# Optimization experiments

Hardware: AMD Instinct MI355X
Metric: run time of the kernel (lower is better)

Reference implementation:

```python
import jax, jax.numpy as jnp
import numpy as np

B, S, E = 2, 2048, 2048
NH, NKV, HD = 32, 8, 64
GS = NH // NKV  # group size = 4
EPS = 1e-6
ROPE_THETA = 10000.0


def setup_inputs() -> dict:
    key = jax.random.key(0)
    ks = jax.random.split(key, 6)
    x = jax.random.normal(ks[0], (B, S, E), jnp.float32)
    position_ids = jnp.broadcast_to(jnp.arange(S, dtype=jnp.int32), (B, S))
    # causal additive mask [1,1,S,S]
    causal = jnp.tril(jnp.ones((S, S), jnp.bool_))
    attn_mask = jnp.where(causal, 0.0, -1e9).astype(jnp.float32)[None, None]
    sc = 0.02
    Wq = jax.random.normal(ks[1], (E, NH * HD), jnp.float32) * sc
    Wk = jax.random.normal(ks[2], (E, NKV * HD), jnp.float32) * sc
    Wv = jax.random.normal(ks[3], (E, NKV * HD), jnp.float32) * sc
    Wo = jax.random.normal(ks[4], (NH * HD, E), jnp.float32) * sc
    q_norm_w = jnp.ones((HD,), jnp.float32)
    k_norm_w = jnp.ones((HD,), jnp.float32)
    return {"x": x, "position_ids": position_ids, "attn_mask": attn_mask,
            "Wq": Wq, "Wk": Wk, "Wv": Wv, "Wo": Wo,
            "q_norm_w": q_norm_w, "k_norm_w": k_norm_w}


def rms_norm(x, w):
    dt = x.dtype
    xf = x.astype(jnp.float32)
    xf = xf * jax.lax.rsqrt(jnp.mean(xf * xf, axis=-1, keepdims=True) + EPS)
    return w * xf.astype(dt)


def apply_rope(x, position_ids):
    # x: [B, H, S, D]; rotate-half RoPE
    D = x.shape[-1]
    inv_freq = 1.0 / (ROPE_THETA ** (jnp.arange(0, D, 2, dtype=jnp.float32) / D))
    freqs = position_ids.astype(jnp.float32)[:, :, None] * inv_freq  # [B,S,D/2]
    cos = jnp.cos(freqs)[:, None]  # [B,1,S,D/2]
    sin = jnp.sin(freqs)[:, None]
    x1, x2 = x[..., : D // 2], x[..., D // 2 :]
    return jnp.concatenate([x1 * cos - x2 * sin, x2 * cos + x1 * sin], axis=-1).astype(x.dtype)


def reference(x, position_ids, attn_mask, Wq, Wk, Wv, Wo, q_norm_w, k_norm_w):
    b, s, _ = x.shape
    Q = (x @ Wq).reshape(b, s, NH, HD).transpose(0, 2, 1, 3)   # [B,NH,S,D]
    K = (x @ Wk).reshape(b, s, NKV, HD).transpose(0, 2, 1, 3)  # [B,NKV,S,D]
    V = (x @ Wv).reshape(b, s, NKV, HD).transpose(0, 2, 1, 3)
    Q = rms_norm(Q, q_norm_w)
    K = rms_norm(K, k_norm_w)
    Q = apply_rope(Q, position_ids)
    K = apply_rope(K, position_ids)
    new_kv_cache = (K, V)
    # GQA: head h attends with kv group h // GS == reshape heads -> (NKV, GS)
    Qg = Q.reshape(b, NKV, GS, s, HD)
    scores = jnp.einsum('bgqsd,bgtd->bgqst', Qg, K) / np.float32(np.sqrt(HD))
    scores = scores + attn_mask[:, :, None]  # broadcast over group dim
    attn = jax.nn.softmax(scores.astype(jnp.float32), axis=-1).astype(x.dtype)
    ctx = jnp.einsum('bgqst,bgtd->bgqsd', attn, V)             # [B,NKV,GS,S,D]
    ctx = ctx.reshape(b, NH, s, HD).transpose(0, 2, 1, 3).reshape(b, s, NH * HD)
    output = ctx @ Wo
    return output, new_kv_cache
```

## Files before the change

### kernel.cpp

```cpp
#include <hip/hip_runtime.h>
#include <stdint.h>

#define S_LEN 2048
#define EMB 2048
#define NHEADS 32
#define NKVH 8
#define HDIM 64

typedef float f32x4 __attribute__((ext_vector_type(4)));
typedef float f32x16 __attribute__((ext_vector_type(16)));
typedef __bf16 bf16x8 __attribute__((ext_vector_type(8)));
typedef unsigned int u32x4 __attribute__((ext_vector_type(4)));

typedef const __attribute__((address_space(1))) void* as1cv;
typedef __attribute__((address_space(3))) void* as3v;

__device__ __forceinline__ void gload_lds16(const void* g, void* l) {
  as1cv gp = (as1cv)(uintptr_t)g;
  as3v lp = (as3v)(uintptr_t)l;
  __builtin_amdgcn_global_load_lds(gp, lp, 16, 0, 0);
}

__device__ __forceinline__ unsigned cvt_pk_bf16(float lo, float hi) {
  unsigned r;
  asm("v_cvt_pk_bf16_f32 %0, %1, %2" : "=v"(r) : "v"(lo), "v"(hi));
  return r;
}

__device__ __forceinline__ void permswap(unsigned& a, unsigned& b) {
  asm("v_permlane32_swap_b32 %0, %1" : "+v"(a), "+v"(b));
}

__device__ __forceinline__ bf16x8 pack4(unsigned a, unsigned b, unsigned c, unsigned d) {
  union { u32x4 u; bf16x8 f; } x;
  x.u = (u32x4){a, b, c, d};
  return x.f;
}

__global__ void rope_table_kernel(float* __restrict__ cosT, float* __restrict__ sinT) {
  int p = blockIdx.x;
  int i = threadIdx.x;
  if (i < 32) {
    float inv = powf(10000.0f, -(float)i / 32.0f);
    float ang = (float)p * inv;
    cosT[p * 32 + i] = cosf(ang);
    sinT[p * 32 + i] = sinf(ang);
  }
}

__global__ __launch_bounds__(256) void cast_bf16_kernel(const float* __restrict__ in,
                                                        __bf16* __restrict__ out, int n8) {
  int i = blockIdx.x * 256 + threadIdx.x;
  if (i < n8) {
    f32x4 a = *(const f32x4*)(in + (size_t)i * 8);
    f32x4 b = *(const f32x4*)(in + (size_t)i * 8 + 4);
    bf16x8 o;
    o[0] = (__bf16)a[0]; o[1] = (__bf16)a[1]; o[2] = (__bf16)a[2]; o[3] = (__bf16)a[3];
    o[4] = (__bf16)b[0]; o[5] = (__bf16)b[1]; o[6] = (__bf16)b[2]; o[7] = (__bf16)b[3];
    *(bf16x8*)(out + (size_t)i * 8) = o;
  }
}

__global__ __launch_bounds__(256) void transpose_cast_kernel(const float* __restrict__ in,
                                                             __bf16* __restrict__ out,
                                                             int R, int C) {
  __shared__ float t[64][65];
  int c0 = blockIdx.x * 64, r0 = blockIdx.y * 64;
  int tid = threadIdx.x;
#pragma unroll
  for (int i = 0; i < 16; ++i) {
    int e = i * 256 + tid;
    int rr = e >> 6, cc = e & 63;
    t[rr][cc] = in[(size_t)(r0 + rr) * C + c0 + cc];
  }
  __syncthreads();
#pragma unroll
  for (int i = 0; i < 16; ++i) {
    int e = i * 256 + tid;
    int rr = e >> 6, cc = e & 63;
    out[(size_t)(c0 + rr) * R + r0 + cc] = (__bf16)t[cc][rr];
  }
}

template <int BM, int BN, typename OUT>
__global__ __launch_bounds__(256, 2) void gemm4w_kernel(const __bf16* __restrict__ A,
                                                        const __bf16* __restrict__ B,
                                                        OUT* __restrict__ C,
                                                        int M, int N, int K) {
  constexpr int MF = (BM / 2) / 16;
  constexpr int NF = (BN / 2) / 16;
  constexpr int ROWS = BM + BN;
  constexpr int NCALL = ROWS / 32;
  constexpr int CHA = BM / 32;
  __shared__ __align__(16) __bf16 sm[2][ROWS * 64];

  const int NT = K >> 6;
  const int nt = N / BN;
  const int nwg = (M / BM) * nt;
  const int q8 = nwg >> 3;
  int wg = blockIdx.x;
  int swz = (wg & 7) * q8 + (wg >> 3);
  int bm = swz / nt, bn = swz % nt;
  size_t m0 = (size_t)bm * BM, n0 = (size_t)bn * BN;

  int tid = threadIdx.x;
  int L = tid & 63, w = tid >> 6;
  int wrow = w >> 1, wcol = w & 1;
  int l15 = L & 15, hi2 = L >> 4;
  int lx = (l15 & 7) << 4;
  const int cx0 = (hi2 << 4) ^ lx;
  const int cx1 = (64 + (hi2 << 4)) ^ lx;

  int srow = tid >> 3;
  int scol = ((tid & 7) ^ (srow & 7)) << 3;
  const __bf16* pA = A + (size_t)(m0 + srow) * K + scol;
  const __bf16* pB = B + (size_t)(n0 + srow) * K + scol;

  char* smb = (char*)sm;
  const int aRow = (wrow * (BM / 2) + l15) * 128;
  const int bRow = (BM + wcol * (BN / 2) + l15) * 128;

  f32x4 acc[MF][NF];
#pragma unroll
  for (int m = 0; m < MF; ++m)
#pragma unroll
    for (int n = 0; n < NF; ++n) acc[m][n] = (f32x4){0.f, 0.f, 0.f, 0.f};

  auto STG = [&](int buf, int c, int t) {
    const __bf16* s = (c < CHA) ? pA + (size_t)(c << 5) * K + ((size_t)t << 6)
                                : pB + (size_t)((c - CHA) << 5) * K + ((size_t)t << 6);
    gload_lds16(s, smb + buf * (ROWS * 128) + c * 4096 + tid * 16);
  };

#pragma unroll
  for (int c = 0; c < NCALL; ++c) STG(0, c, 0);
#pragma unroll
  for (int c = 0; c < NCALL; ++c) STG(1, c, 1);
  if constexpr (NCALL == 10) asm volatile("s_waitcnt vmcnt(10)" ::: "memory");
  else asm volatile("s_waitcnt vmcnt(8)" ::: "memory");
  __builtin_amdgcn_s_barrier();

  for (int t = 0; t < NT; ++t) {
    const char* aC = smb + (t & 1) * (ROWS * 128);
    bf16x8 af[MF][2], bf[NF][2];
#pragma unroll
    for (int n = 0; n < NF; ++n) {
      bf[n][0] = *(const bf16x8*)(aC + bRow + n * 2048 + cx0);
      bf[n][1] = *(const bf16x8*)(aC + bRow + n * 2048 + cx1);
    }
#pragma unroll
    for (int m = 0; m < MF; ++m) {
      af[m][0] = *(const bf16x8*)(aC + aRow + m * 2048 + cx0);
      af[m][1] = *(const bf16x8*)(aC + aRow + m * 2048 + cx1);
    }
    asm volatile("s_waitcnt lgkmcnt(4)" ::: "memory");
    __builtin_amdgcn_sched_barrier(0);
    __builtin_amdgcn_s_setprio(1);
#pragma unroll
    for (int m = 0; m < MF / 2; ++m)
#pragma unroll
      for (int n = 0; n < NF; ++n)
#pragma unroll
        for (int kk = 0; kk < 2; ++kk)
          acc[m][n] = __builtin_amdgcn_mfma_f32_16x16x32_bf16(
              kk ? af[m][1] : af[m][0], kk ? bf[n][1] : bf[n][0], acc[m][n], 0, 0, 0);
    __builtin_amdgcn_s_setprio(0);
    asm volatile("s_waitcnt lgkmcnt(0)" ::: "memory");
    __builtin_amdgcn_sched_barrier(0);
    __builtin_amdgcn_s_barrier();
    if (t + 2 < NT) {
#pragma unroll
      for (int c = 0; c < NCALL; ++c) STG(t & 1, c, t + 2);
    }
    __builtin_amdgcn_s_setprio(1);
#pragma unroll
    for (int m = MF / 2; m < MF; ++m)
#pragma unroll
      for (int n = 0; n < NF; ++n)
#pragma unroll
        for (int kk = 0; kk < 2; ++kk)
          acc[m][n] = __builtin_amdgcn_mfma_f32_16x16x32_bf16(
              kk ? af[m][1] : af[m][0], kk ? bf[n][1] : bf[n][0], acc[m][n], 0, 0, 0);
    __builtin_amdgcn_s_setprio(0);
    if (t + 2 < NT) {
      if constexpr (NCALL == 10) asm volatile("s_waitcnt vmcnt(10)" ::: "memory");
      else asm volatile("s_waitcnt vmcnt(8)" ::: "memory");
    } else if (t + 1 < NT) {
      asm volatile("s_waitcnt vmcnt(0)" ::: "memory");
    }
    __builtin_amdgcn_s_barrier();
  }

#pragma unroll
  for (int m = 0; m < MF; ++m)
#pragma unroll
    for (int n = 0; n < NF; ++n)
#pragma unroll
      for (int r = 0; r < 4; ++r)
        C[(m0 + wrow * (BM / 2) + m * 16 + (hi2 << 2) + r) * (size_t)N + n0 +
          wcol * (BN / 2) + n * 16 + l15] = (OUT)acc[m][n][r];
}

__global__ __launch_bounds__(256) void rmsrope_kernel(
    const __bf16* __restrict__ QKV, const int* __restrict__ pos,
    const float* __restrict__ qw, const float* __restrict__ kw,
    const float* __restrict__ cosT, const float* __restrict__ sinT,
    __bf16* __restrict__ Qatt, __bf16* __restrict__ Katt, __bf16* __restrict__ Vtatt,
    float* __restrict__ Kc, float* __restrict__ Vc) {
  int token = blockIdx.x;
  int b = token >> 11, s = token & 2047;
  int tid = threadIdx.x, lane = tid & 63, wid = tid >> 6;
  int p = pos[token];
  int i = lane & 31;
  float cs = cosT[p * 32 + i], sn = sinT[p * 32 + i];
  const __bf16* base = QKV + (size_t)token * 3072;
  float qwl = qw[lane], kwl = kw[lane];
  const float qscale = 0.18033688011112042f;

  for (int h = wid; h < NHEADS; h += 4) {
    float v = (float)base[h * 64 + lane];
    float ss = v * v;
#pragma unroll
    for (int m = 1; m < 64; m <<= 1) ss += __shfl_xor(ss, m);
    float xn = v * rsqrtf(ss * (1.0f / 64.0f) + 1e-6f) * qwl;
    float other = __shfl_xor(xn, 32);
    float o = xn * cs + ((lane < 32) ? -other * sn : other * sn);
    Qatt[((size_t)(b * NHEADS + h) * S_LEN + s) * HDIM + lane] = (__bf16)(o * qscale);
  }
  for (int g = wid; g < NKVH; g += 4) {
    float v = (float)base[2048 + g * 64 + lane];
    float ss = v * v;
#pragma unroll
    for (int m = 1; m < 64; m <<= 1) ss += __shfl_xor(ss, m);
    float xn = v * rsqrtf(ss * (1.0f / 64.0f) + 1e-6f) * kwl;
    float other = __shfl_xor(xn, 32);
    float o = xn * cs + ((lane < 32) ? -other * sn : other * sn);
    size_t kidx = ((size_t)(b * NKVH + g) * S_LEN + s) * HDIM + lane;
    Katt[kidx] = (__bf16)o;
    Kc[kidx] = o;
  }
  for (int g = wid; g < NKVH; g += 4) {
    float v = (float)base[2560 + g * 64 + lane];
    size_t vidx = ((size_t)(b * NKVH + g) * S_LEN + s) * HDIM + lane;
    Vc[vidx] = v;
    Vtatt[((size_t)(b * NKVH + g) * HDIM + lane) * S_LEN + s] = (__bf16)v;
  }
}

__global__ __launch_bounds__(256, 2) void attn_kernel(const __bf16* __restrict__ Qatt,
                                                      const __bf16* __restrict__ Katt,
                                                      const __bf16* __restrict__ Vtatt,
                                                      __bf16* __restrict__ ctx) {
  __shared__ __align__(16) __bf16 Ks[2][4096];
  __shared__ __align__(16) __bf16 Vs[2][4096];
  int bid = blockIdx.x;
  int qt, bg;
  if (bid < 256) { qt = 31 - (bid >> 4); bg = bid & 15; }
  else { qt = (bid - 256) >> 4; bg = bid & 15; }
  int b = bg >> 3, g = bg & 7;
  int tid = threadIdx.x, lane = tid & 63, w = tid >> 6;
  int l31 = lane & 31, hi = lane >> 5;
  int h = g * 4 + w;

  const __bf16* Kg = Katt + (size_t)bg * (S_LEN * HDIM);
  const __bf16* Vg = Vtatt + (size_t)bg * (HDIM * S_LEN);
  const __bf16* Qg = Qatt + ((size_t)(b * NHEADS + h) * S_LEN + qt * 64 + l31) * HDIM;

  bf16x8 qf0[4], qf1[4];
#pragma unroll
  for (int ds = 0; ds < 4; ++ds) {
    qf0[ds] = *(const bf16x8*)(Qg + ds * 16 + (hi << 3));
    qf1[ds] = *(const bf16x8*)(Qg + 32 * HDIM + ds * 16 + (hi << 3));
  }

  f32x16 acc00, acc01, acc10, acc11;
#pragma unroll
  for (int r = 0; r < 16; ++r) { acc00[r] = 0.f; acc01[r] = 0.f; acc10[r] = 0.f; acc11[r] = 0.f; }
  float l0 = 0.f, l1 = 0.f;

  int sr = tid >> 3;
  int sc = ((tid & 7) ^ (sr & 7)) << 3;
  const __bf16* Ksrc = Kg + (size_t)sr * HDIM + sc;
  const __bf16* Vsrc = Vg + (size_t)sr * S_LEN + sc;

  gload_lds16(Ksrc, &Ks[0][tid * 8]);
  gload_lds16(Ksrc + 32 * HDIM, &Ks[0][2048 + tid * 8]);
  gload_lds16(Vsrc, &Vs[0][tid * 8]);
  gload_lds16(Vsrc + (size_t)32 * S_LEN, &Vs[0][2048 + tid * 8]);
  __syncthreads();

  int rx = (l31 & 7) << 4;

  for (int t = 0; t <= qt; ++t) {
    int cur = t & 1;
    if (t < qt) {
      const __bf16* kn = Ksrc + (size_t)(t + 1) * (64 * HDIM);
      const __bf16* vn = Vsrc + (size_t)(t + 1) * 64;
      gload_lds16(kn, &Ks[cur ^ 1][tid * 8]);
      gload_lds16(kn + 32 * HDIM, &Ks[cur ^ 1][2048 + tid * 8]);
      gload_lds16(vn, &Vs[cur ^ 1][tid * 8]);
      gload_lds16(vn + (size_t)32 * S_LEN, &Vs[cur ^ 1][2048 + tid * 8]);
    }
    f32x16 s00, s01, s10, s11;
#pragma unroll
    for (int r = 0; r < 16; ++r) { s00[r] = 0.f; s01[r] = 0.f; s10[r] = 0.f; s11[r] = 0.f; }
    {
      const char* kb0 = (const char*)Ks[cur] + (size_t)l31 * 128;
      const char* kb1 = kb0 + 4096;
#pragma unroll
      for (int dstep = 0; dstep < 4; ++dstep) {
        int cb = dstep * 32 + (hi << 4);
        bf16x8 k0 = *(const bf16x8*)(kb0 + (cb ^ rx));
        bf16x8 k1 = *(const bf16x8*)(kb1 + (cb ^ rx));
        s00 = __builtin_amdgcn_mfma_f32_32x32x16_bf16(k0, qf0[dstep], s00, 0, 0, 0);
        s01 = __builtin_amdgcn_mfma_f32_32x32x16_bf16(k1, qf0[dstep], s01, 0, 0, 0);
        s10 = __builtin_amdgcn_mfma_f32_32x32x16_bf16(k0, qf1[dstep], s10, 0, 0, 0);
        s11 = __builtin_amdgcn_mfma_f32_32x32x16_bf16(k1, qf1[dstep], s11, 0, 0, 0);
      }
    }
    if (t == qt) {
#pragma unroll
      for (int r = 0; r < 16; ++r) {
        int kb = (r & 3) + 8 * (r >> 2) + (hi << 2);
        if (kb > l31) { s00[r] = -3e38f; s11[r] = -3e38f; }
        s01[r] = -3e38f;
      }
    }
#pragma unroll
    for (int r = 0; r < 16; ++r) {
      s00[r] = __builtin_amdgcn_exp2f(s00[r]);
      s01[r] = __builtin_amdgcn_exp2f(s01[r]);
      s10[r] = __builtin_amdgcn_exp2f(s10[r]);
      s11[r] = __builtin_amdgcn_exp2f(s11[r]);
    }
    {
      float a0 = 0.f, a1 = 0.f, a2 = 0.f, a3 = 0.f;
      float b0 = 0.f, b1 = 0.f, b2 = 0.f, b3 = 0.f;
#pragma unroll
      for (int r = 0; r < 16; r += 4) {
        a0 += s00[r]; a1 += s00[r + 1]; a2 += s00[r + 2]; a3 += s00[r + 3];
        a0 += s01[r]; a1 += s01[r + 1]; a2 += s01[r + 2]; a3 += s01[r + 3];
        b0 += s10[r]; b1 += s10[r + 1]; b2 += s10[r + 2]; b3 += s10[r + 3];
        b0 += s11[r]; b1 += s11[r + 1]; b2 += s11[r + 2]; b3 += s11[r + 3];
      }
      l0 += (a0 + a1) + (a2 + a3);
      l1 += (b0 + b1) + (b2 + b3);
    }
    bf16x8 pf0[4], pf1[4];
    {
      unsigned wd[8];
#pragma unroll
      for (int i = 0; i < 8; ++i) wd[i] = cvt_pk_bf16(s00[2 * i], s00[2 * i + 1]);
      permswap(wd[0], wd[2]); permswap(wd[1], wd[3]);
      permswap(wd[4], wd[6]); permswap(wd[5], wd[7]);
      pf0[0] = pack4(wd[0], wd[1], wd[2], wd[3]);
      pf0[1] = pack4(wd[4], wd[5], wd[6], wd[7]);
#pragma unroll
      for (int i = 0; i < 8; ++i) wd[i] = cvt_pk_bf16(s01[2 * i], s01[2 * i + 1]);
      permswap(wd[0], wd[2]); permswap(wd[1], wd[3]);
      permswap(wd[4], wd[6]); permswap(wd[5], wd[7]);
      pf0[2] = pack4(wd[0], wd[1], wd[2], wd[3]);
      pf0[3] = pack4(wd[4], wd[5], wd[6], wd[7]);
#pragma unroll
      for (int i = 0; i < 8; ++i) wd[i] = cvt_pk_bf16(s10[2 * i], s10[2 * i + 1]);
      permswap(wd[0], wd[2]); permswap(wd[1], wd[3]);
      permswap(wd[4], wd[6]); permswap(wd[5], wd[7]);
      pf1[0] = pack4(wd[0], wd[1], wd[2], wd[3]);
      pf1[1] = pack4(wd[4], wd[5], wd[6], wd[7]);
#pragma unroll
      for (int i = 0; i < 8; ++i) wd[i] = cvt_pk_bf16(s11[2 * i], s11[2 * i + 1]);
      permswap(wd[0], wd[2]); permswap(wd[1], wd[3]);
      permswap(wd[4], wd[6]); permswap(wd[5], wd[7]);
      pf1[2] = pack4(wd[0], wd[1], wd[2], wd[3]);
      pf1[3] = pack4(wd[4], wd[5], wd[6], wd[7]);
    }
    {
      const char* vb0 = (const char*)Vs[cur] + (size_t)l31 * 128;
      const char* vb1 = vb0 + 4096;
#pragma unroll
      for (int ks = 0; ks < 4; ++ks) {
        int cb = ks * 32 + (hi << 4);
        bf16x8 v0 = *(const bf16x8*)(vb0 + (cb ^ rx));
        bf16x8 v1 = *(const bf16x8*)(vb1 + (cb ^ rx));
        acc00 = __builtin_amdgcn_mfma_f32_32x32x16_bf16(v0, pf0[ks], acc00, 0, 0, 0);
        acc01 = __builtin_amdgcn_mfma_f32_32x32x16_bf16(v1, pf0[ks], acc01, 0, 0, 0);
        acc10 = __builtin_amdgcn_mfma_f32_32x32x16_bf16(v0, pf1[ks], acc10, 0, 0, 0);
        acc11 = __builtin_amdgcn_mfma_f32_32x32x16_bf16(v1, pf1[ks], acc11, 0, 0, 0);
      }
    }
    __syncthreads();
  }

  l0 += __shfl_xor(l0, 32);
  l1 += __shfl_xor(l1, 32);
  float inv0 = 1.f / l0, inv1 = 1.f / l1;
  size_t orow0 = ((size_t)(b * S_LEN + qt * 64 + l31)) * EMB + h * HDIM;
  size_t orow1 = orow0 + (size_t)32 * EMB;
#pragma unroll
  for (int r = 0; r < 16; r += 2) {
    int d = (r & 3) + 8 * (r >> 2) + (hi << 2);
    unsigned w00 = cvt_pk_bf16(acc00[r] * inv0, acc00[r + 1] * inv0);
    unsigned w01 = cvt_pk_bf16(acc01[r] * inv0, acc01[r + 1] * inv0);
    unsigned w10 = cvt_pk_bf16(acc10[r] * inv1, acc10[r + 1] * inv1);
    unsigned w11 = cvt_pk_bf16(acc11[r] * inv1, acc11[r + 1] * inv1);
    *(unsigned*)((char*)ctx + (orow0 + d) * 2) = w00;
    *(unsigned*)((char*)ctx + (orow0 + 32 + d) * 2) = w01;
    *(unsigned*)((char*)ctx + (orow1 + d) * 2) = w10;
    *(unsigned*)((char*)ctx + (orow1 + 32 + d) * 2) = w11;
  }
}

extern "C" void kernel_launch(void* const* d_in, const int* in_sizes, int n_in,
                              void* d_out, int out_size, void* d_ws, size_t ws_size,
                              hipStream_t stream) {
  const float* x = (const float*)d_in[0];
  const int* pos = (const int*)d_in[1];
  const float* Wq = (const float*)d_in[3];
  const float* Wk = (const float*)d_in[4];
  const float* Wv = (const float*)d_in[5];
  const float* Wo = (const float*)d_in[6];
  const float* qw = (const float*)d_in[7];
  const float* kw = (const float*)d_in[8];

  float* out = (float*)d_out;
  float* Kc = out + (size_t)2 * 2048 * 2048;
  float* Vc = Kc + (size_t)2 * 8 * 2048 * 64;

  char* ws = (char*)d_ws;
  size_t off = 0;
  auto alloc = [&](size_t bytes) {
    char* p = ws + off;
    off += (bytes + 255) & ~(size_t)255;
    return (void*)p;
  };
  __bf16* xb = (__bf16*)alloc((size_t)4096 * 2048 * 2);
  __bf16* Wcat = (__bf16*)alloc((size_t)3072 * 2048 * 2);
  __bf16* Wot = (__bf16*)alloc((size_t)2048 * 2048 * 2);
  __bf16* QKV = (__bf16*)alloc((size_t)4096 * 3072 * 2);
  __bf16* ctx = (__bf16*)alloc((size_t)4096 * 2048 * 2);
  __bf16* Qatt = (__bf16*)alloc((size_t)2 * 32 * 2048 * 64 * 2);
  __bf16* Katt = (__bf16*)alloc((size_t)2 * 8 * 2048 * 64 * 2);
  __bf16* Vtat = (__bf16*)alloc((size_t)2 * 8 * 2048 * 64 * 2);
  float* cosT = (float*)alloc((size_t)2048 * 32 * 4);
  float* sinT = (float*)alloc((size_t)2048 * 32 * 4);

  rope_table_kernel<<<2048, 64, 0, stream>>>(cosT, sinT);
  cast_bf16_kernel<<<4096, 256, 0, stream>>>(x, xb, 4096 * 2048 / 8);
  transpose_cast_kernel<<<dim3(32, 32), 256, 0, stream>>>(Wq, Wcat, 2048, 2048);
  transpose_cast_kernel<<<dim3(8, 32), 256, 0, stream>>>(Wk, Wcat + (size_t)2048 * 2048, 2048, 512);
  transpose_cast_kernel<<<dim3(8, 32), 256, 0, stream>>>(Wv, Wcat + (size_t)2560 * 2048, 2048, 512);
  transpose_cast_kernel<<<dim3(32, 32), 256, 0, stream>>>(Wo, Wot, 2048, 2048);
  gemm4w_kernel<128, 192, __bf16><<<512, 256, 0, stream>>>(xb, Wcat, QKV, 4096, 3072, 2048);
  rmsrope_kernel<<<4096, 256, 0, stream>>>(QKV, pos, qw, kw, cosT, sinT, Qatt, Katt, Vtat, Kc, Vc);
  attn_kernel<<<512, 256, 0, stream>>>(Qatt, Katt, Vtat, ctx);
  gemm4w_kernel<128, 128, float><<<512, 256, 0, stream>>>(ctx, Wot, out, 4096, 2048, 2048);
}
```

Before: 186.2 us.

## Split long causal attention tiles across two KV chunks with a combine pass

The attention grid grows from 512 to 768 blocks. The 16 longest query tiles per batch-group split their KV range into two halves, each written as unnormalized bf16 partial output plus row sums, and a new combine kernel adds the halves and normalizes into ctx. This aims to reduce tail imbalance from causal masking, where the longest tiles dominate runtime. It also wraps the MFMA loops in s_setprio. The cost is an extra kernel launch, partial-buffer traffic, and a bf16 rounding of partials before they are combined.

```diff
diff --git a/kernel.cpp b/kernel.cpp
--- a/kernel.cpp
+++ b/kernel.cpp
@@ -250,17 +250,27 @@
 __global__ __launch_bounds__(256, 2) void attn_kernel(const __bf16* __restrict__ Qatt,
                                                       const __bf16* __restrict__ Katt,
                                                       const __bf16* __restrict__ Vtatt,
-                                                      __bf16* __restrict__ ctx) {
+                                                      __bf16* __restrict__ ctx,
+                                                      __bf16* __restrict__ Opart,
+                                                      float* __restrict__ lpart) {
   __shared__ __align__(16) __bf16 Ks[2][4096];
   __shared__ __align__(16) __bf16 Vs[2][4096];
   int bid = blockIdx.x;
-  int qt, bg;
-  if (bid < 256) { qt = 31 - (bid >> 4); bg = bid & 15; }
-  else { qt = (bid - 256) >> 4; bg = bid & 15; }
+  int c = bid >> 4, bg = bid & 15;
+  int qt, t0, t1, qi, chunk;
+  if (c < 32) {
+    qt = 31 - (c >> 1); chunk = c & 1; qi = 31 - qt;
+    int nh = (qt + 2) >> 1;
+    t0 = chunk ? nh : 0;
+    t1 = chunk ? (qt + 1) : nh;
+  } else {
+    qt = 47 - c; chunk = 0; qi = -1; t0 = 0; t1 = qt + 1;
+  }
   int b = bg >> 3, g = bg & 7;
   int tid = threadIdx.x, lane = tid & 63, w = tid >> 6;
   int l31 = lane & 31, hi = lane >> 5;
   int h = g * 4 + w;
+  int rx = (l31 & 7) << 4;
 
   const __bf16* Kg = Katt + (size_t)bg * (S_LEN * HDIM);
   const __bf16* Vg = Vtatt + (size_t)bg * (HDIM * S_LEN);
@@ -283,30 +293,31 @@
   const __bf16* Ksrc = Kg + (size_t)sr * HDIM + sc;
   const __bf16* Vsrc = Vg + (size_t)sr * S_LEN + sc;
 
-  gload_lds16(Ksrc, &Ks[0][tid * 8]);
-  gload_lds16(Ksrc + 32 * HDIM, &Ks[0][2048 + tid * 8]);
-  gload_lds16(Vsrc, &Vs[0][tid * 8]);
-  gload_lds16(Vsrc + (size_t)32 * S_LEN, &Vs[0][2048 + tid * 8]);
+  auto STAGE = [&](int buf, int t) {
+    const __bf16* kt = Ksrc + (size_t)t * (64 * HDIM);
+    const __bf16* vt = Vsrc + (size_t)t * 64;
+    gload_lds16(kt, &Ks[buf][tid * 8]);
+    gload_lds16(kt + 32 * HDIM, &Ks[buf][2048 + tid * 8]);
+    gload_lds16(vt, &Vs[buf][tid * 8]);
+    gload_lds16(vt + (size_t)32 * S_LEN, &Vs[buf][2048 + tid * 8]);
+  };
+
+  STAGE(0, t0);
   __syncthreads();
 
-  int rx = (l31 & 7) << 4;
-
-  for (int t = 0; t <= qt; ++t) {
-    int cur = t & 1;
-    if (t < qt) {
-      const __bf16* kn = Ksrc + (size_t)(t + 1) * (64 * HDIM);
-      const __bf16* vn = Vsrc + (size_t)(t + 1) * 64;
-      gload_lds16(kn, &Ks[cur ^ 1][tid * 8]);
-      gload_lds16(kn + 32 * HDIM, &Ks[cur ^ 1][2048 + tid * 8]);
-      gload_lds16(vn, &Vs[cur ^ 1][tid * 8]);
-      gload_lds16(vn + (size_t)32 * S_LEN, &Vs[cur ^ 1][2048 + tid * 8]);
-    }
+  int niter = t1 - t0;
+#pragma unroll 1
+  for (int i = 0; i < niter; ++i) {
+    int cur = i & 1;
+    int t = t0 + i;
+    if (i + 1 < niter) STAGE(cur ^ 1, t + 1);
     f32x16 s00, s01, s10, s11;
 #pragma unroll
     for (int r = 0; r < 16; ++r) { s00[r] = 0.f; s01[r] = 0.f; s10[r] = 0.f; s11[r] = 0.f; }
     {
       const char* kb0 = (const char*)Ks[cur] + (size_t)l31 * 128;
       const char* kb1 = kb0 + 4096;
+      __builtin_amdgcn_s_setprio(1);
 #pragma unroll
       for (int dstep = 0; dstep < 4; ++dstep) {
         int cb = dstep * 32 + (hi << 4);
@@ -317,6 +328,7 @@
         s10 = __builtin_amdgcn_mfma_f32_32x32x16_bf16(k0, qf1[dstep], s10, 0, 0, 0);
         s11 = __builtin_amdgcn_mfma_f32_32x32x16_bf16(k1, qf1[dstep], s11, 0, 0, 0);
       }
+      __builtin_amdgcn_s_setprio(0);
     }
     if (t == qt) {
 #pragma unroll
@@ -350,25 +362,25 @@
     {
       unsigned wd[8];
 #pragma unroll
-      for (int i = 0; i < 8; ++i) wd[i] = cvt_pk_bf16(s00[2 * i], s00[2 * i + 1]);
+      for (int q = 0; q < 8; ++q) wd[q] = cvt_pk_bf16(s00[2 * q], s00[2 * q + 1]);
       permswap(wd[0], wd[2]); permswap(wd[1], wd[3]);
       permswap(wd[4], wd[6]); permswap(wd[5], wd[7]);
       pf0[0] = pack4(wd[0], wd[1], wd[2], wd[3]);
       pf0[1] = pack4(wd[4], wd[5], wd[6], wd[7]);
 #pragma unroll
-      for (int i = 0; i < 8; ++i) wd[i] = cvt_pk_bf16(s01[2 * i], s01[2 * i + 1]);
+      for (int q = 0; q < 8; ++q) wd[q] = cvt_pk_bf16(s01[2 * q], s01[2 * q + 1]);
       permswap(wd[0], wd[2]); permswap(wd[1], wd[3]);
       permswap(wd[4], wd[6]); permswap(wd[5], wd[7]);
       pf0[2] = pack4(wd[0], wd[1], wd[2], wd[3]);
       pf0[3] = pack4(wd[4], wd[5], wd[6], wd[7]);
 #pragma unroll
-      for (int i = 0; i < 8; ++i) wd[i] = cvt_pk_bf16(s10[2 * i], s10[2 * i + 1]);
+      for (int q = 0; q < 8; ++q) wd[q] = cvt_pk_bf16(s10[2 * q], s10[2 * q + 1]);
       permswap(wd[0], wd[2]); permswap(wd[1], wd[3]);
       permswap(wd[4], wd[6]); permswap(wd[5], wd[7]);
       pf1[0] = pack4(wd[0], wd[1], wd[2], wd[3]);
       pf1[1] = pack4(wd[4], wd[5], wd[6], wd[7]);
 #pragma unroll
-      for (int i = 0; i < 8; ++i) wd[i] = cvt_pk_bf16(s11[2 * i], s11[2 * i + 1]);
+      for (int q = 0; q < 8; ++q) wd[q] = cvt_pk_bf16(s11[2 * q], s11[2 * q + 1]);
       permswap(wd[0], wd[2]); permswap(wd[1], wd[3]);
       permswap(wd[4], wd[6]); permswap(wd[5], wd[7]);
       pf1[2] = pack4(wd[0], wd[1], wd[2], wd[3]);
@@ -377,6 +389,7 @@
     {
       const char* vb0 = (const char*)Vs[cur] + (size_t)l31 * 128;
       const char* vb1 = vb0 + 4096;
+      __builtin_amdgcn_s_setprio(1);
 #pragma unroll
       for (int ks = 0; ks < 4; ++ks) {
         int cb = ks * 32 + (hi << 4);
@@ -387,26 +400,65 @@
         acc10 = __builtin_amdgcn_mfma_f32_32x32x16_bf16(v0, pf1[ks], acc10, 0, 0, 0);
         acc11 = __builtin_amdgcn_mfma_f32_32x32x16_bf16(v1, pf1[ks], acc11, 0, 0, 0);
       }
+      __builtin_amdgcn_s_setprio(0);
     }
     __syncthreads();
   }
 
   l0 += __shfl_xor(l0, 32);
   l1 += __shfl_xor(l1, 32);
-  float inv0 = 1.f / l0, inv1 = 1.f / l1;
-  size_t orow0 = ((size_t)(b * S_LEN + qt * 64 + l31)) * EMB + h * HDIM;
-  size_t orow1 = orow0 + (size_t)32 * EMB;
-#pragma unroll
-  for (int r = 0; r < 16; r += 2) {
-    int d = (r & 3) + 8 * (r >> 2) + (hi << 2);
-    unsigned w00 = cvt_pk_bf16(acc00[r] * inv0, acc00[r + 1] * inv0);
-    unsigned w01 = cvt_pk_bf16(acc01[r] * inv0, acc01[r + 1] * inv0);
-    unsigned w10 = cvt_pk_bf16(acc10[r] * inv1, acc10[r + 1] * inv1);
-    unsigned w11 = cvt_pk_bf16(acc11[r] * inv1, acc11[r + 1] * inv1);
-    *(unsigned*)((char*)ctx + (orow0 + d) * 2) = w00;
-    *(unsigned*)((char*)ctx + (orow0 + 32 + d) * 2) = w01;
-    *(unsigned*)((char*)ctx + (orow1 + d) * 2) = w10;
-    *(unsigned*)((char*)ctx + (orow1 + 32 + d) * 2) = w11;
+  if (qi < 0) {
+    float inv0 = 1.f / l0, inv1 = 1.f / l1;
+    size_t orow0 = ((size_t)(b * S_LEN + qt * 64 + l31)) * EMB + h * HDIM;
+    size_t orow1 = orow0 + (size_t)32 * EMB;
+#pragma unroll
+    for (int r = 0; r < 16; r += 2) {
+      int d = (r & 3) + 8 * (r >> 2) + (hi << 2);
+      unsigned w00 = cvt_pk_bf16(acc00[r] * inv0, acc00[r + 1] * inv0);
+      unsigned w01 = cvt_pk_bf16(acc01[r] * inv0, acc01[r + 1] * inv0);
+      unsigned w10 = cvt_pk_bf16(acc10[r] * inv1, acc10[r + 1] * inv1);
+      unsigned w11 = cvt_pk_bf16(acc11[r] * inv1, acc11[r + 1] * inv1);
+      *(unsigned*)((char*)ctx + (orow0 + d) * 2) = w00;
+      *(unsigned*)((char*)ctx + (orow0 + 32 + d) * 2) = w01;
+      *(unsigned*)((char*)ctx + (orow1 + d) * 2) = w10;
+      *(unsigned*)((char*)ctx + (orow1 + 32 + d) * 2) = w11;
+    }
+  } else {
+    int pidx = (bg * 16 + qi) * 2 + chunk;
+    __bf16* ob = Opart + ((size_t)pidx * 4 + w) * 4096;
+#pragma unroll
+    for (int r = 0; r < 16; r += 2) {
+      int d = (r & 3) + 8 * (r >> 2) + (hi << 2);
+      *(unsigned*)((char*)ob + (l31 * 64 + d) * 2) = cvt_pk_bf16(acc00[r], acc00[r + 1]);
+      *(unsigned*)((char*)ob + (l31 * 64 + 32 + d) * 2) = cvt_pk_bf16(acc01[r], acc01[r + 1]);
+      *(unsigned*)((char*)ob + ((32 + l31) * 64 + d) * 2) = cvt_pk_bf16(acc10[r], acc10[r + 1]);
+      *(unsigned*)((char*)ob + ((32 + l31) * 64 + 32 + d) * 2) = cvt_pk_bf16(acc11[r], acc11[r + 1]);
+    }
+    if (hi == 0) {
+      lpart[pidx * 256 + w * 64 + l31] = l0;
+      lpart[pidx * 256 + w * 64 + 32 + l31] = l1;
+    }
+  }
+}
+
+__global__ __launch_bounds__(256) void attn_combine_kernel(const __bf16* __restrict__ Opart,
+                                                           const float* __restrict__ lpart,
+                                                           __bf16* __restrict__ ctx) {
+  int bid = blockIdx.x;
+  int hq = bid & 3, qi = (bid >> 2) & 15, bg = bid >> 6;
+  int b = bg >> 3, g = bg & 7, h = g * 4 + hq;
+  int qt = 31 - qi;
+  int t = threadIdx.x, d = t & 63, q0 = t >> 6;
+  int p = (bg * 16 + qi) * 2;
+  const __bf16* o0 = Opart + ((size_t)p * 4 + hq) * 4096;
+  const __bf16* o1 = o0 + 4 * 4096;
+  const float* la = lpart + p * 256 + hq * 64;
+  const float* lb = la + 256;
+#pragma unroll
+  for (int q = q0; q < 64; q += 4) {
+    float o = (float)o0[q * 64 + d] + (float)o1[q * 64 + d];
+    float inv = 1.f / (la[q] + lb[q]);
+    ctx[((size_t)(b * S_LEN + qt * 64 + q)) * EMB + h * 64 + d] = (__bf16)(o * inv);
   }
 }
 
@@ -443,6 +495,8 @@
   __bf16* Vtat = (__bf16*)alloc((size_t)2 * 8 * 2048 * 64 * 2);
   float* cosT = (float*)alloc((size_t)2048 * 32 * 4);
   float* sinT = (float*)alloc((size_t)2048 * 32 * 4);
+  __bf16* Opart = (__bf16*)alloc((size_t)512 * 4 * 4096 * 2);
+  float* lpart = (float*)alloc((size_t)512 * 256 * 4);
 
   rope_table_kernel<<<2048, 64, 0, stream>>>(cosT, sinT);
   cast_bf16_kernel<<<4096, 256, 0, stream>>>(x, xb, 4096 * 2048 / 8);
@@ -452,6 +506,7 @@
   transpose_cast_kernel<<<dim3(32, 32), 256, 0, stream>>>(Wo, Wot, 2048, 2048);
   gemm4w_kernel<128, 192, __bf16><<<512, 256, 0, stream>>>(xb, Wcat, QKV, 4096, 3072, 2048);
   rmsrope_kernel<<<4096, 256, 0, stream>>>(QKV, pos, qw, kw, cosT, sinT, Qatt, Katt, Vtat, Kc, Vc);
-  attn_kernel<<<512, 256, 0, stream>>>(Qatt, Katt, Vtat, ctx);
+  attn_kernel<<<768, 256, 0, stream>>>(Qatt, Katt, Vtat, ctx, Opart, lpart);
+  attn_combine_kernel<<<1024, 256, 0, stream>>>(Opart, lpart, ctx);
   gemm4w_kernel<128, 128, float><<<512, 256, 0, stream>>>(ctx, Wot, out, 4096, 2048, 2048);
 }
```

Measured after the change: 201.4 us. 1.08x slower.
